# Performance work log

Hardware: AMD Instinct MI355X
Metric: run time of the kernel (lower is better)

The kernel has to match this reference:

```python
import jax, jax.numpy as jnp
import numpy as np

B = 32768
NUM_SPARSE = 26
VOCAB = 100000
EMB = 128
DENSE_IN = 13
N_FIELDS = NUM_SPARSE + 1  # 27
INTER_DIM = N_FIELDS * (N_FIELDS - 1) // 2  # 351
TOP_IN = EMB + INTER_DIM  # 479


def setup_inputs() -> dict:
    key = jax.random.key(0)
    ks = jax.random.split(key, 12)
    inp = {
        "dense_x": jax.random.normal(ks[0], (B, DENSE_IN), dtype=jnp.float32),
        "sparse_x": jax.random.randint(ks[1], (B, NUM_SPARSE), 0, VOCAB, dtype=jnp.int64),
        # embedding tables stacked: [F, V, D]
        "emb_tables": jax.random.normal(ks[2], (NUM_SPARSE, VOCAB, EMB), dtype=jnp.float32) * 0.02,
        # bottom MLP: dense_in -> 256 -> emb
        "bw1": jax.random.normal(ks[3], (DENSE_IN, 256), dtype=jnp.float32) * 0.1,
        "bb1": jnp.zeros((256,), dtype=jnp.float32),
        "bw2": jax.random.normal(ks[4], (256, EMB), dtype=jnp.float32) * 0.05,
        "bb2": jnp.zeros((EMB,), dtype=jnp.float32),
        # top MLP: top_in -> 128 -> 64 -> 1
        "tw1": jax.random.normal(ks[5], (TOP_IN, 128), dtype=jnp.float32) * 0.05,
        "tb1": jnp.zeros((128,), dtype=jnp.float32),
        "tw2": jax.random.normal(ks[6], (128, 64), dtype=jnp.float32) * 0.1,
        "tb2": jnp.zeros((64,), dtype=jnp.float32),
        "tw3": jax.random.normal(ks[7], (64, 1), dtype=jnp.float32) * 0.1,
        "tb3": jnp.zeros((1,), dtype=jnp.float32),
    }
    return inp


def reference(dense_x, sparse_x, emb_tables, bw1, bb1, bw2, bb2,
              tw1, tb1, tw2, tb2, tw3, tb3):
    # bottom MLP
    h = jax.nn.relu(dense_x @ bw1 + bb1)
    x_bottom = jax.nn.relu(h @ bw2 + bb2)  # [B, EMB]

    # multi-table embedding gather: [B, F_sparse, EMB]
    field_idx = jnp.arange(NUM_SPARSE)[None, :]  # [1, F]
    sparse_embs = emb_tables[field_idx, sparse_x]  # [B, F, EMB]

    combined = jnp.concatenate([x_bottom[:, None, :], sparse_embs], axis=1)  # [B, 27, EMB]

    # pairwise dot interactions, take strict upper triangle
    interactions = jnp.einsum("bfd,bgd->bfg", combined, combined)  # [B, 27, 27]
    rows, cols = np.triu_indices(N_FIELDS, k=1)
    x_int = interactions[:, rows, cols]  # [B, 351]

    x_final = jnp.concatenate([x_bottom, x_int], axis=-1)  # [B, 479]

    # top MLP
    t = jax.nn.relu(x_final @ tw1 + tb1)
    t = jax.nn.relu(t @ tw2 + tb2)
    logits = t @ tw3 + tb3  # [B, 1]
    return jax.nn.sigmoid(logits)
```

## Files before the change

### kernel.cpp

```cpp
#include <hip/hip_runtime.h>
#include <hip/hip_bf16.h>
#include <stdint.h>

#define NUM_SPARSE 26
#define VOCAB 100000
#define EMB 128
#define ROWS 32

typedef __attribute__((ext_vector_type(8))) short bf16x8;
typedef __attribute__((ext_vector_type(16))) float f32x16;

__device__ __forceinline__ unsigned short f2bf(float x) {
    union { float f; uint32_t u; } v; v.f = x;
    uint32_t u = v.u;
    return (unsigned short)((u + 0x7FFFu + ((u >> 16) & 1u)) >> 16);
}
__device__ __forceinline__ uint32_t pack2bf(float a, float b) {
    __hip_bfloat162 h2 = __float22bfloat162_rn(float2{a, b});
    union { __hip_bfloat162 h; uint32_t u; } v; v.h = h2;
    return v.u;
}

__device__ __forceinline__ int swz(int r, int c, int rowbytes) {
    int b = 2 * c;
    return r * rowbytes + (((b >> 4) ^ (r & 15)) << 4) + (b & 15);
}
__device__ __forceinline__ bf16x8 ldsA(const char* base, int m, int k0, int rowbytes) {
    int slot = (k0 >> 3) ^ (m & 15);
    return *(const bf16x8*)(base + m * rowbytes + slot * 16);
}

__global__ void prep_weights(const float* __restrict__ bw2, const float* __restrict__ tw1,
                             const float* __restrict__ tw2, unsigned short* __restrict__ ws) {
    int i = blockIdx.x * blockDim.x + threadIdx.x;
    if (i < 128 * 256) {
        int n = i >> 8, k = i & 255;
        ws[i] = f2bf(bw2[k * 128 + n]);
    } else if (i < 128 * 256 + 128 * 480) {
        int j = i - 128 * 256;
        int n = j / 480, k = j - n * 480;
        ws[i] = f2bf(k < 479 ? tw1[k * 128 + n] : 0.f);
    } else if (i < 128 * 256 + 128 * 480 + 64 * 128) {
        int j = i - (128 * 256 + 128 * 480);
        int n = j >> 7, k = j & 127;
        ws[i] = f2bf(tw2[k * 64 + n]);
    }
}

#define GATHER(row, BUF)                                                               \
    {                                                                                  \
        _Pragma("unroll") for (int i = 0; i < 13; i++) {                               \
            int fld = 2 * i + hi;                                                      \
            int idx = __shfl(idxs[row], fld);                                          \
            BUF[i] = *(const float4*)(emb + ((size_t)fld * VOCAB + (size_t)idx) * EMB  \
                                      + 4 * lm);                                       \
        }                                                                              \
    }

#define CONSUME(ri, BUF)                                                               \
    {                                                                                  \
        int r = w * 8 + (ri);                                                          \
        {                                                                              \
            uint32_t v = *(const uint32_t*)(xf + swz(r, 2 * l, 1024));                 \
            *(uint32_t*)(Cb + 4 * l) = v;     \
        }                                                                              \
        _Pragma("unroll") for (int i = 0; i < 13; i++) {                               \
            int frow = 1 + 2 * i + hi;                                                 \
            uint32_t p0 = pack2bf(BUF[i].x, BUF[i].y);                                 \
            uint32_t p1 = pack2bf(BUF[i].z, BUF[i].w);                                 \
            char* dst = Cb + frow * 256 + ((((lm >> 1) ^ (frow & 15))) << 4)           \
                        + (lm & 1) * 8;                                                \
            *(uint32_t*)dst = p0;                                                      \
            *(uint32_t*)(dst + 4) = p1;                                                \
        }                                                                              \
        f32x16 acc = {0,0,0,0,0,0,0,0,0,0,0,0,0,0,0,0};                                \
        _Pragma("unroll") for (int kk = 0; kk < 8; kk++) {                             \
            int k0 = kk * 16 + hi * 8;                                                 \
            bf16x8 a = ldsA(Cb, lm, k0, 256);                                          \
            acc = __builtin_amdgcn_mfma_f32_32x32x16_bf16(a, a, acc, 0, 0, 0);         \
        }                                                                              \
        int n = lm;                                                                    \
        if (n >= 1 && n <= 26) {                                                       \
            _Pragma("unroll") for (int reg = 0; reg < 16; reg++) {                     \
                int m = (reg & 3) + 8 * (reg >> 2) + 4 * hi;                           \
                if (m < n) {                                                           \
                    int p = 26 * m - (m * (m - 1)) / 2 + (n - m - 1);                  \
                    *(unsigned short*)(xf + swz(r, 128 + p, 1024)) = f2bf(acc[reg]);   \
                }                                                                      \
            }                                                                          \
        }                                                                              \
    }

__global__ __launch_bounds__(256, 2) void dlrm_main(
    const float* __restrict__ dense, const int* __restrict__ sparse,
    const float* __restrict__ emb, const float* __restrict__ bw1,
    const float* __restrict__ bb1, const float* __restrict__ bb2,
    const float* __restrict__ tb1, const float* __restrict__ tb2,
    const float* __restrict__ tw3, const float* __restrict__ tb3,
    const unsigned short* __restrict__ wsw, float* __restrict__ out)
{
    __shared__ __align__(16) char smem[65536];
    const int t = threadIdx.x;
    const int w = t >> 6;
    const int l = t & 63;
    const int hi = l >> 5;
    const int lm = l & 31;
    const int r0 = blockIdx.x * ROWS;

    float* xd = (float*)smem;
    char* xf = smem + 32768;
    char* Cb = smem + w * 8192;

    int idxs[8];
#pragma unroll
    for (int ri = 0; ri < 8; ri++)
        idxs[ri] = (l < NUM_SPARSE)
            ? sparse[(size_t)(r0 + w * 8 + ri) * NUM_SPARSE + l] : 0;

    for (int i = t; i < ROWS * 13; i += 256) xd[i] = dense[r0 * 13 + i];
    for (int i = t; i < ROWS * 33; i += 256) {
        int r = i / 33, c = 479 + (i - r * 33);
        *(unsigned short*)(xf + swz(r, c, 1024)) = 0;
    }

    float4 bufA[13], bufB[13], bufC[13];
    GATHER(0, bufA);
    GATHER(1, bufB);
    __syncthreads();

    {
        char* hb = smem + 2048;
        int j = t;
        float w1r[13];
#pragma unroll
        for (int k = 0; k < 13; k++) w1r[k] = bw1[k * 256 + j];
        float b = bb1[j];
        for (int r = 0; r < ROWS; r++) {
            float acc = b;
#pragma unroll
            for (int k = 0; k < 13; k++) acc += xd[r * 13 + k] * w1r[k];
            *(unsigned short*)(hb + swz(r, j, 512)) = f2bf(fmaxf(acc, 0.f));
        }
    }
    __syncthreads();

    {
        const char* hb = smem + 2048;
        const unsigned short* bw2t = wsw;
        int n0 = w * 32;
        f32x16 acc = {0,0,0,0,0,0,0,0,0,0,0,0,0,0,0,0};
#pragma unroll
        for (int kk = 0; kk < 16; kk++) {
            int k0 = kk * 16 + hi * 8;
            bf16x8 a = ldsA(hb, lm, k0, 512);
            bf16x8 b = *(const bf16x8*)(bw2t + (n0 + lm) * 256 + k0);
            acc = __builtin_amdgcn_mfma_f32_32x32x16_bf16(a, b, acc, 0, 0, 0);
        }
        float bias = bb2[n0 + lm];
#pragma unroll
        for (int reg = 0; reg < 16; reg++) {
            int m = (reg & 3) + 8 * (reg >> 2) + 4 * hi;
            float v = fmaxf(acc[reg] + bias, 0.f);
            *(unsigned short*)(xf + swz(m, n0 + lm, 1024)) = f2bf(v);
        }
    }
    __syncthreads();

    GATHER(2, bufC); CONSUME(0, bufA);
    GATHER(3, bufA); CONSUME(1, bufB);
    GATHER(4, bufB); CONSUME(2, bufC);
    GATHER(5, bufC); CONSUME(3, bufA);
    GATHER(6, bufA); CONSUME(4, bufB);
    GATHER(7, bufB); CONSUME(5, bufC);
    CONSUME(6, bufA);
    CONSUME(7, bufB);
    __syncthreads();

    {
        const unsigned short* tw1t = wsw + 32768;
        int n0 = w * 32;
        f32x16 acc = {0,0,0,0,0,0,0,0,0,0,0,0,0,0,0,0};
#pragma unroll
        for (int kk = 0; kk < 30; kk++) {
            int k0 = kk * 16 + hi * 8;
            bf16x8 a = ldsA(xf, lm, k0, 1024);
            bf16x8 b = *(const bf16x8*)(tw1t + (n0 + lm) * 480 + k0);
            acc = __builtin_amdgcn_mfma_f32_32x32x16_bf16(a, b, acc, 0, 0, 0);
        }
        float bias = tb1[n0 + lm];
#pragma unroll
        for (int reg = 0; reg < 16; reg++) {
            int m = (reg & 3) + 8 * (reg >> 2) + 4 * hi;
            float v = fmaxf(acc[reg] + bias, 0.f);
            *(unsigned short*)(smem + swz(m, n0 + lm, 256)) = f2bf(v);
        }
    }
    __syncthreads();

    float* t2b = (float*)(smem + 8192);
    if (w < 2) {
        const unsigned short* tw2t = wsw + 32768 + 61440;
        int n0 = w * 32;
        f32x16 acc = {0,0,0,0,0,0,0,0,0,0,0,0,0,0,0,0};
#pragma unroll
        for (int kk = 0; kk < 8; kk++) {
            int k0 = kk * 16 + hi * 8;
            bf16x8 a = ldsA(smem, lm, k0, 256);
            bf16x8 b = *(const bf16x8*)(tw2t + (n0 + lm) * 128 + k0);
            acc = __builtin_amdgcn_mfma_f32_32x32x16_bf16(a, b, acc, 0, 0, 0);
        }
        float bias = tb2[n0 + lm];
#pragma unroll
        for (int reg = 0; reg < 16; reg++) {
            int m = (reg & 3) + 8 * (reg >> 2) + 4 * hi;
            t2b[m * 65 + n0 + lm] = fmaxf(acc[reg] + bias, 0.f);
        }
    }
    __syncthreads();

    if (t < ROWS) {
        float acc = tb3[0];
#pragma unroll
        for (int k = 0; k < 64; k++) acc += t2b[t * 65 + k] * tw3[k];
        out[r0 + t] = 1.f / (1.f + expf(-acc));
    }
}

extern "C" void kernel_launch(void* const* d_in, const int* in_sizes, int n_in,
                              void* d_out, int out_size, void* d_ws, size_t ws_size,
                              hipStream_t stream) {
    const float* dense = (const float*)d_in[0];
    const int*   sparse = (const int*)d_in[1];
    const float* emb   = (const float*)d_in[2];
    const float* bw1   = (const float*)d_in[3];
    const float* bb1   = (const float*)d_in[4];
    const float* bw2   = (const float*)d_in[5];
    const float* bb2   = (const float*)d_in[6];
    const float* tw1   = (const float*)d_in[7];
    const float* tb1   = (const float*)d_in[8];
    const float* tw2   = (const float*)d_in[9];
    const float* tb2   = (const float*)d_in[10];
    const float* tw3   = (const float*)d_in[11];
    const float* tb3   = (const float*)d_in[12];
    unsigned short* wsw = (unsigned short*)d_ws;
    float* out = (float*)d_out;

    hipLaunchKernelGGL(prep_weights, dim3(400), dim3(256), 0, stream, bw2, tw1, tw2, wsw);
    hipLaunchKernelGGL(dlrm_main, dim3(32768 / ROWS), dim3(256), 0, stream,
                       dense, sparse, emb, bw1, bb1, bb2, tb1, tb2, tw3, tb3, wsw, out);
}
```

Before: 112.7 us.

## Shrink gather pipeline to double buffering and coalesce weight prep reads

```diff
diff --git a/kernel.cpp b/kernel.cpp
--- a/kernel.cpp
+++ b/kernel.cpp
@@ -33,17 +33,20 @@
 __global__ void prep_weights(const float* __restrict__ bw2, const float* __restrict__ tw1,
                              const float* __restrict__ tw2, unsigned short* __restrict__ ws) {
     int i = blockIdx.x * blockDim.x + threadIdx.x;
-    if (i < 128 * 256) {
-        int n = i >> 8, k = i & 255;
-        ws[i] = f2bf(bw2[k * 128 + n]);
-    } else if (i < 128 * 256 + 128 * 480) {
-        int j = i - 128 * 256;
-        int n = j / 480, k = j - n * 480;
-        ws[i] = f2bf(k < 479 ? tw1[k * 128 + n] : 0.f);
-    } else if (i < 128 * 256 + 128 * 480 + 64 * 128) {
-        int j = i - (128 * 256 + 128 * 480);
-        int n = j >> 7, k = j & 127;
-        ws[i] = f2bf(tw2[k * 64 + n]);
+    if (i < 256 * 128) {
+        int k = i >> 7, n = i & 127;
+        ws[n * 256 + k] = f2bf(bw2[i]);
+    } else if (i < 256 * 128 + 479 * 128) {
+        int j = i - 256 * 128;
+        int k = j >> 7, n = j & 127;
+        ws[32768 + n * 480 + k] = f2bf(tw1[j]);
+    } else if (i < 256 * 128 + 479 * 128 + 128) {
+        int n = i - (256 * 128 + 479 * 128);
+        ws[32768 + n * 480 + 479] = 0;
+    } else if (i < 256 * 128 + 479 * 128 + 128 + 128 * 64) {
+        int j = i - (256 * 128 + 479 * 128 + 128);
+        int k = j >> 6, n = j & 63;
+        ws[94208 + n * 128 + k] = f2bf(tw2[j]);
     }
 }
 
@@ -123,7 +126,7 @@
         *(unsigned short*)(xf + swz(r, c, 1024)) = 0;
     }
 
-    float4 bufA[13], bufB[13], bufC[13];
+    float4 bufA[13], bufB[13];
     GATHER(0, bufA);
     GATHER(1, bufB);
     __syncthreads();
@@ -166,12 +169,12 @@
     }
     __syncthreads();
 
-    GATHER(2, bufC); CONSUME(0, bufA);
-    GATHER(3, bufA); CONSUME(1, bufB);
-    GATHER(4, bufB); CONSUME(2, bufC);
-    GATHER(5, bufC); CONSUME(3, bufA);
-    GATHER(6, bufA); CONSUME(4, bufB);
-    GATHER(7, bufB); CONSUME(5, bufC);
+    CONSUME(0, bufA); GATHER(2, bufA);
+    CONSUME(1, bufB); GATHER(3, bufB);
+    CONSUME(2, bufA); GATHER(4, bufA);
+    CONSUME(3, bufB); GATHER(5, bufB);
+    CONSUME(4, bufA); GATHER(6, bufA);
+    CONSUME(5, bufB); GATHER(7, bufB);
     CONSUME(6, bufA);
     CONSUME(7, bufB);
     __syncthreads();
```

New measurement: 101.9 us. 9.6% less time.
